# Kernel tuning notes

Hardware: AMD Instinct MI355X
Metric: run time of the kernel (lower is better)

The kernel has to match this reference:

```python
import jax, jax.numpy as jnp
import numpy as np

N = 100_000      # nodes
E = 1_600_000    # edges (avg degree 16)
IN = 512         # in_feats
HID = 4          # hidden_feats (forced equal to num_heads=4 by the mean(h,2) in forward)
H1 = 4           # heads in layer 1
OUT = 128        # out_feats
NEG_SLOPE = 0.2  # DGL GATConv leaky_relu default


def setup_inputs() -> dict:
    key = jax.random.key(0)
    ks = jax.random.split(key, 12)
    nfeats = jax.random.normal(ks[0], (N, IN), jnp.float32)
    efeats = jax.random.normal(ks[1], (E, 8), jnp.float32)  # unused by the module
    src = jax.random.randint(ks[2], (E,), 0, N, dtype=jnp.int32)
    dst = jax.random.randint(ks[3], (E,), 0, N, dtype=jnp.int32)
    # layer 1 params (in=IN, heads=H1, per-head out=HID)
    fc1_w = jax.random.normal(ks[4], (IN, H1 * HID), jnp.float32) / np.sqrt(IN)
    attn_l1 = jax.random.normal(ks[5], (H1, HID), jnp.float32) / np.sqrt(HID)
    attn_r1 = jax.random.normal(ks[6], (H1, HID), jnp.float32) / np.sqrt(HID)
    bias1 = jnp.zeros((H1 * HID,), jnp.float32)
    # layer 2 params (in=H1=4 after mean over feature dim, heads=1, out=OUT)
    fc2_w = jax.random.normal(ks[7], (HID, 1 * OUT), jnp.float32) / np.sqrt(HID)
    attn_l2 = jax.random.normal(ks[8], (1, OUT), jnp.float32) / np.sqrt(OUT)
    attn_r2 = jax.random.normal(ks[9], (1, OUT), jnp.float32) / np.sqrt(OUT)
    bias2 = jnp.zeros((OUT,), jnp.float32)
    return {"nfeats": nfeats, "efeats": efeats, "src": src, "dst": dst,
            "fc1_w": fc1_w, "attn_l1": attn_l1, "attn_r1": attn_r1, "bias1": bias1,
            "fc2_w": fc2_w, "attn_l2": attn_l2, "attn_r2": attn_r2, "bias2": bias2}


def gat_layer(x, src, dst, fc_w, attn_l, attn_r, bias, heads, d_out):
    # projection: (N, in) -> (N, H, D)
    h = (x @ fc_w).reshape(-1, heads, d_out)
    el = jnp.einsum('nhd,hd->nh', h, attn_l)   # (N, H)
    er = jnp.einsum('nhd,hd->nh', h, attn_r)
    e = jax.nn.leaky_relu(el[src] + er[dst], NEG_SLOPE)  # (E, H)
    # segment softmax over incoming edges of each dst node
    m = jax.lax.stop_gradient(jax.ops.segment_max(e, dst, num_segments=N))
    ex = jnp.exp(e - m[dst])
    denom = jax.ops.segment_sum(ex, dst, num_segments=N)
    alpha = ex / denom[dst]                    # (E, H)
    msg = alpha[:, :, None] * h[src]           # (E, H, D)
    rst = jax.ops.segment_sum(msg, dst, num_segments=N)  # (N, H, D)
    return rst + bias.reshape(1, heads, d_out)


def reference(nfeats, efeats, src, dst, fc1_w, attn_l1, attn_r1, bias1,
              fc2_w, attn_l2, attn_r2, bias2):
    h = gat_layer(nfeats, src, dst, fc1_w, attn_l1, attn_r1, bias1, H1, HID)  # (N,4,4)
    h = jnp.mean(h, axis=2)        # faithful to th.mean(h, 2): mean over per-head feat dim -> (N,4)
    h = jax.nn.relu(h)
    h = gat_layer(h, src, dst, fc2_w, attn_l2, attn_r2, bias2, 1, OUT)        # (N,1,OUT)
    return h.reshape(N, OUT)       # flatten(1)
```

## Files before the change

kernel.cpp:

```cpp
#include <hip/hip_runtime.h>
#include <math.h>

#define IN_F 512
#define OUTF 128
#define NEG_SLOPE 0.2f

typedef __attribute__((ext_vector_type(8))) short bf16x8;
typedef __attribute__((ext_vector_type(4))) float f32x4;

#define P1T 256
#define XP 136
#define NKS 16
#define BPSH 8192

#define NPB 128
#define NBMAX 784
#define EPB 4096
#define SRCMASK 0x1FFFF
#define CAP 2944

#define BP_BYTES (2 * BPSH * 2)
#define XS_BYTES (4 * 16 * XP * 2)
#define SMEM_A   (BP_BYTES + XS_BYTES)

__device__ __forceinline__ unsigned pkbf(float a, float b) {
  unsigned ua = __float_as_uint(a); ua += 0x7FFF + ((ua >> 16) & 1);
  unsigned ub = __float_as_uint(b); ub += 0x7FFF + ((ub >> 16) & 1);
  return (ua >> 16) | (ub & 0xFFFF0000u);
}

__global__ void k_prep(const float* __restrict__ fc1, const float* __restrict__ al1,
                       const float* __restrict__ ar1, const float* __restrict__ fc2,
                       const float* __restrict__ al2, const float* __restrict__ ar2,
                       unsigned short* __restrict__ BpHi, unsigned short* __restrict__ BpLo,
                       float* __restrict__ w2al, float* __restrict__ w2ar,
                       int* __restrict__ bucketCursor) {
  __shared__ float wlds[IN_F * 12];
  int t = threadIdx.x;
  if (blockIdx.x == 0) {
    int k = t;
#pragma unroll
    for (int h = 0; h < 4; ++h) {
      float wl = 0.f, wr = 0.f, wb = 0.f;
#pragma unroll
      for (int j = 0; j < 4; ++j) {
        float wv = fc1[k * 16 + h * 4 + j];
        wl = fmaf(wv, al1[h * 4 + j], wl);
        wr = fmaf(wv, ar1[h * 4 + j], wr);
        wb += wv;
      }
      wlds[k * 12 + h] = wl;
      wlds[k * 12 + 4 + h] = wr;
      wlds[k * 12 + 8 + h] = 0.25f * wb;
    }
    __syncthreads();
    for (int item = t; item < NKS * 64; item += 512) {
      int s = item >> 6, l = item & 63;
      int col = l & 15;
      int kb = s * 32 + ((l >> 4) * 8);
      unsigned hi[4], lo[4];
#pragma unroll
      for (int p = 0; p < 4; ++p) {
        float w0 = 0.f, w1 = 0.f;
        if (col < 12) {
          w0 = wlds[(kb + 2 * p) * 12 + col];
          w1 = wlds[(kb + 2 * p + 1) * 12 + col];
        }
        unsigned u0 = __float_as_uint(w0); u0 += 0x7FFF + ((u0 >> 16) & 1);
        unsigned u1 = __float_as_uint(w1); u1 += 0x7FFF + ((u1 >> 16) & 1);
        unsigned h0 = u0 >> 16, h1 = u1 >> 16;
        hi[p] = h0 | (h1 << 16);
        float r0 = w0 - __uint_as_float(h0 << 16);
        float r1 = w1 - __uint_as_float(h1 << 16);
        lo[p] = pkbf(r0, r1);
      }
      *(uint4*)&BpHi[item * 8] = make_uint4(hi[0], hi[1], hi[2], hi[3]);
      *(uint4*)&BpLo[item * 8] = make_uint4(lo[0], lo[1], lo[2], lo[3]);
    }
  } else {
    if (t < 8) {
      int h = t >> 1;
      const float* a = (t & 1) ? ar2 : al2;
      float s = 0.f;
#pragma unroll 16
      for (int c = 0; c < OUTF; ++c) s += fc2[h * OUTF + c] * a[c];
      if (t & 1) w2ar[h] = s; else w2al[h] = s;
    }
    for (int i = t; i < NBMAX; i += 512) bucketCursor[i] = 0;
  }
}

__global__ __launch_bounds__(P1T) void k_A(
    const float* __restrict__ x,
    const unsigned short* __restrict__ BpHi, const unsigned short* __restrict__ BpLo,
    float* __restrict__ pk1, float* __restrict__ er1, int n,
    const int* __restrict__ src, const int* __restrict__ dst,
    int* __restrict__ bucketCursor, unsigned* __restrict__ ep, int e,
    int projBlocks)
{
  __shared__ __align__(16) char smem[SMEM_A];
  const int t = threadIdx.x;

  if ((int)blockIdx.x < projBlocks) {
    const int lane = t & 63;
    const int wv = t >> 6;
    const bf16x8* Bfrag = (const bf16x8*)smem;
    short* xsw = (short*)(smem + BP_BYTES) + wv * (16 * XP);

    for (int i = t; i < 2 * NKS * 64; i += P1T) {
      ((uint4*)smem)[i] = (i < NKS * 64) ? ((const uint4*)BpHi)[i]
                                         : ((const uint4*)BpLo)[i - NKS * 64];
    }
    __syncthreads();

    const int totalWaves = projBlocks * 4;
    const int rtMax = (n + 15) >> 4;
    for (int rt = blockIdx.x * 4 + wv; rt < rtMax; rt += totalWaves) {
      const int wrow = rt * 16;
      const float* __restrict__ xr = x + (size_t)wrow * IN_F;
      f32x4 acc = {0.f, 0.f, 0.f, 0.f};

      float4 st[8];
#pragma unroll
      for (int i = 0; i < 8; ++i) {
        int f = lane + i * 64;
        int r = f >> 5, c4 = (f & 31) * 4;
        st[i] = (wrow + r < n) ? *(const float4*)&xr[(size_t)r * IN_F + c4]
                               : make_float4(0.f, 0.f, 0.f, 0.f);
      }

      for (int kt = 0; kt < 4; ++kt) {
#pragma unroll
        for (int i = 0; i < 8; ++i) {
          int f = lane + i * 64;
          int r = f >> 5, c4 = (f & 31) * 4;
          uint2 pv; pv.x = pkbf(st[i].x, st[i].y); pv.y = pkbf(st[i].z, st[i].w);
          *(uint2*)&xsw[r * XP + c4] = pv;
        }
        if (kt < 3) {
          int kb = (kt + 1) * 128;
#pragma unroll
          for (int i = 0; i < 8; ++i) {
            int f = lane + i * 64;
            int r = f >> 5, c4 = (f & 31) * 4;
            st[i] = (wrow + r < n) ? *(const float4*)&xr[(size_t)r * IN_F + kb + c4]
                                   : make_float4(0.f, 0.f, 0.f, 0.f);
          }
        }
        asm volatile("s_waitcnt lgkmcnt(0)" ::: "memory");
        __builtin_amdgcn_sched_barrier(0);
#pragma unroll
        for (int ks = 0; ks < 4; ++ks) {
          bf16x8 a = *(const bf16x8*)&xsw[(lane & 15) * XP + ks * 32 + ((lane >> 4) * 8)];
          int bidx = (kt * 4 + ks) * 64 + lane;
          bf16x8 bh = Bfrag[bidx];
          bf16x8 bl = Bfrag[NKS * 64 + bidx];
          acc = __builtin_amdgcn_mfma_f32_16x16x32_bf16(a, bh, acc, 0, 0, 0);
          acc = __builtin_amdgcn_mfma_f32_16x16x32_bf16(a, bl, acc, 0, 0, 0);
        }
      }

      int col = lane & 15;
      int rbase = wrow + ((lane >> 4) * 4);
#pragma unroll
      for (int i = 0; i < 4; ++i) {
        int row = rbase + i;
        if (row < n) {
          float v = acc[i];
          if (col < 4)       pk1[(size_t)row * 8 + col] = v;
          else if (col < 8)  er1[(size_t)row * 4 + (col - 4)] = v;
          else if (col < 12) pk1[(size_t)row * 8 + 4 + (col - 8)] = v;
        }
      }
    }
  } else {
    int* hist = (int*)smem;
    int* base = hist + NBMAX;
    int* lcur = base + NBMAX;
    const int bb = blockIdx.x - projBlocks;
    for (int i = t; i < NBMAX; i += P1T) hist[i] = 0;
    __syncthreads();
    int blockBase = bb * EPB;
#pragma unroll
    for (int i = 0; i < EPB / P1T; ++i) {
      int idx = blockBase + t + i * P1T;
      if (idx < e) atomicAdd(&hist[dst[idx] >> 7], 1);
    }
    __syncthreads();
    for (int i = t; i < NBMAX; i += P1T) {
      if (hist[i] > 0) base[i] = atomicAdd(&bucketCursor[i], hist[i]);
      lcur[i] = 0;
    }
    __syncthreads();
#pragma unroll
    for (int i = 0; i < EPB / P1T; ++i) {
      int idx = blockBase + t + i * P1T;
      if (idx < e) {
        int d = dst[idx];
        int b = d >> 7;
        int off = base[b] + atomicAdd(&lcur[b], 1);
        if (off < CAP)
          ep[(size_t)b * CAP + off] = (unsigned)src[idx] | ((unsigned)(d & (NPB - 1)) << 17);
      }
    }
  }
}

__global__ __launch_bounds__(256) void k_B(
    const unsigned* __restrict__ ep, const int* __restrict__ bucketCursor,
    unsigned* __restrict__ ep2, int* __restrict__ nodeBeg, int* __restrict__ nodeEnd,
    const float* __restrict__ pk1, const float* __restrict__ er1,
    const float* __restrict__ bias1,
    const float* __restrict__ w2al, const float* __restrict__ w2ar,
    float* __restrict__ pk2, float* __restrict__ er2, int n)
{
  __shared__ int cnt[NPB];
  __shared__ int scn[NPB];
  __shared__ int cur[NPB];
  __shared__ unsigned lbuf[CAP];
  int t = threadIdx.x;
  int b = blockIdx.x;
  int nodeBase = b * NPB;
  int m = bucketCursor[b];
  if (m > CAP) m = CAP;
  const unsigned* __restrict__ in = ep + (size_t)b * CAP;
  if (t < NPB) cnt[t] = 0;
  __syncthreads();
  for (int j = t; j < m; j += 256) atomicAdd(&cnt[in[j] >> 17], 1);
  __syncthreads();
  if (t < NPB) scn[t] = cnt[t];
  __syncthreads();
  for (int off = 1; off < NPB; off <<= 1) {
    int v = (t < NPB && t >= off) ? scn[t - off] : 0;
    __syncthreads();
    if (t < NPB) scn[t] += v;
    __syncthreads();
  }
  if (t < NPB) {
    int excl = scn[t] - cnt[t];
    int node = nodeBase + t;
    if (node < n) {
      nodeBeg[node] = b * CAP + excl;
      nodeEnd[node] = b * CAP + excl + cnt[t];
    }
    cur[t] = excl;
  }
  __syncthreads();
  for (int j = t; j < m; j += 256) {
    unsigned p = in[j];
    int pos = atomicAdd(&cur[p >> 17], 1);
    lbuf[pos] = p & SRCMASK;
  }
  __syncthreads();
  for (int i = t; i < m; i += 256) ep2[(size_t)b * CAP + i] = lbuf[i];

#pragma unroll
  for (int half = 0; half < 2; ++half) {
    int w = t + half * 256;
    int i = w >> 2, h = w & 3;
    int node = nodeBase + i;
    bool active = node < n;
    float v = 0.f;
    if (active) {
      int beg = scn[i] - cnt[i], end = scn[i];
      float ern = er1[(size_t)node * 4 + h];
      float den = 0.f, num = 0.f;
      for (int j = beg; j < end; ++j) {
        int s = (int)lbuf[j];
        float el = pk1[(size_t)s * 8 + h];
        float hb = pk1[(size_t)s * 8 + 4 + h];
        float eh = el + ern;
        eh = (eh > 0.f) ? eh : NEG_SLOPE * eh;
        float wg = __expf(eh);
        den += wg;
        num = fmaf(wg, hb, num);
      }
      float mb = 0.25f * (bias1[h*4] + bias1[h*4+1] + bias1[h*4+2] + bias1[h*4+3]);
      v = (end > beg) ? num / den : 0.f;
      v += mb;
      v = (v > 0.f) ? v : 0.f;
    }
    float pl = v * w2al[h];
    float pr = v * w2ar[h];
    pl += __shfl_xor(pl, 1); pl += __shfl_xor(pl, 2);
    pr += __shfl_xor(pr, 1); pr += __shfl_xor(pr, 2);
    if (active) {
      pk2[(size_t)node * 8 + h] = v;
      if (h == 0) { pk2[(size_t)node * 8 + 4] = pl; er2[node] = pr; }
    }
  }
}

__global__ __launch_bounds__(256) void k_bagg2(
    const unsigned* __restrict__ ep2, const int* __restrict__ nodeBeg,
    const int* __restrict__ nodeEnd,
    const float* __restrict__ pk2, const float* __restrict__ er2,
    const float* __restrict__ w2, const float* __restrict__ bias2,
    float* __restrict__ out, int n)
{
  __shared__ float gacc[256 * 4];
  __shared__ float w2s[4 * OUTF];
  __shared__ float b2s[OUTF];
  int t = threadIdx.x;
  int nodeBase = blockIdx.x * 256;
  int nn = nodeBase + t;
  for (int i = t; i < 4 * OUTF; i += 256) w2s[i] = w2[i];
  if (t < OUTF) b2s[t] = bias2[t];
  float g0 = 0.f, g1 = 0.f, g2 = 0.f, g3 = 0.f;
  if (nn < n) {
    int beg = nodeBeg[nn], end = nodeEnd[nn];
    float ern = er2[nn];
    float den = 0.f;
    for (int j = beg; j < end; ++j) {
      int s = (int)ep2[j];
      const float* __restrict__ ps = &pk2[(size_t)s * 8];
      float4 hv = *(const float4*)ps;
      float e = ps[4] + ern;
      e = (e > 0.f) ? e : NEG_SLOPE * e;
      float w = __expf(e);
      den += w;
      g0 = fmaf(w, hv.x, g0); g1 = fmaf(w, hv.y, g1);
      g2 = fmaf(w, hv.z, g2); g3 = fmaf(w, hv.w, g3);
    }
    float inv = (end > beg) ? 1.0f / den : 0.f;
    g0 *= inv; g1 *= inv; g2 *= inv; g3 *= inv;
  }
  gacc[t * 4 + 0] = g0; gacc[t * 4 + 1] = g1;
  gacc[t * 4 + 2] = g2; gacc[t * 4 + 3] = g3;
  __syncthreads();
  for (int idx = t; idx < 256 * (OUTF / 2); idx += 256) {
    int i = idx >> 6;
    int node = nodeBase + i;
    if (node >= n) continue;
    int c = (idx & 63) * 2;
    float gx = gacc[i*4], gy = gacc[i*4+1], gz = gacc[i*4+2], gw = gacc[i*4+3];
    float2 o;
    o.x = gx*w2s[c]   + gy*w2s[OUTF+c]   + gz*w2s[2*OUTF+c]   + gw*w2s[3*OUTF+c]   + b2s[c];
    o.y = gx*w2s[c+1] + gy*w2s[OUTF+c+1] + gz*w2s[2*OUTF+c+1] + gw*w2s[3*OUTF+c+1] + b2s[c+1];
    *(float2*)&out[(size_t)node * OUTF + c] = o;
  }
}

extern "C" void kernel_launch(void* const* d_in, const int* in_sizes, int n_in,
                              void* d_out, int out_size, void* d_ws, size_t ws_size,
                              hipStream_t stream) {
  const float* nfeats = (const float*)d_in[0];
  const int*   srcp   = (const int*)d_in[2];
  const int*   dstp   = (const int*)d_in[3];
  const float* fc1    = (const float*)d_in[4];
  const float* al1    = (const float*)d_in[5];
  const float* ar1    = (const float*)d_in[6];
  const float* bias1  = (const float*)d_in[7];
  const float* fc2    = (const float*)d_in[8];
  const float* al2    = (const float*)d_in[9];
  const float* ar2    = (const float*)d_in[10];
  const float* bias2  = (const float*)d_in[11];

  const int N = in_sizes[0] / IN_F;
  const int E = in_sizes[2];
  const int NB = (N + NPB - 1) / NPB;

  float* ws   = (float*)d_ws;
  float* pk1  = ws;
  float* er1  = pk1 + (size_t)8 * N;
  float* pk2  = er1 + (size_t)4 * N;
  float* er2  = pk2 + (size_t)8 * N;
  float* w2al = er2 + N;
  float* w2ar = w2al + 4;
  unsigned short* BpHi = (unsigned short*)(w2ar + 4);
  unsigned short* BpLo = BpHi + BPSH;
  int* bucketCursor = (int*)(BpLo + BPSH);
  int* nodeBeg      = bucketCursor + NBMAX;
  int* nodeEnd      = nodeBeg + N;
  unsigned* ep      = (unsigned*)(nodeEnd + N);
  unsigned* ep2     = ep + (size_t)NB * CAP;

  const int binBlocks = (E + EPB - 1) / EPB;
  const int projBlocks = 391;

  k_prep<<<2, 512, 0, stream>>>(fc1, al1, ar1, fc2, al2, ar2,
                                BpHi, BpLo, w2al, w2ar, bucketCursor);
  k_A<<<projBlocks + binBlocks, P1T, 0, stream>>>(nfeats, BpHi, BpLo, pk1, er1, N,
                                                  srcp, dstp, bucketCursor, ep, E,
                                                  projBlocks);
  k_B<<<NB, 256, 0, stream>>>(ep, bucketCursor, ep2, nodeBeg, nodeEnd,
                              pk1, er1, bias1, w2al, w2ar, pk2, er2, N);
  k_bagg2<<<(N + 255) / 256, 256, 0, stream>>>(ep2, nodeBeg, nodeEnd, pk2, er2,
                                               fc2, bias2, (float*)d_out, N);
}
```

Measured before the change: 135.3 us.

## Load MFMA A-fragments directly from global memory, drop LDS staging of x

The projection GEMM no longer stages converted x tiles through a per-wave LDS buffer. Each lane now loads its own 8-float slice of its row directly from global memory into registers, using a 4-deep register prefetch ring, then packs it to bf16 and feeds the MFMA. This removes the LDS writes, LDS reads and waitcnt barriers, and shrinks shared memory, which could raise occupancy. The trade-off is that global loads become less coalesced: each row is read in 32-byte pieces with a 2 KB stride between lanes instead of in contiguous rows.

New measurement: 198.1 us. +46.5%, slower.

```diff
diff --git a/kernel.cpp b/kernel.cpp
--- a/kernel.cpp
+++ b/kernel.cpp
@@ -7,10 +7,11 @@
 
 typedef __attribute__((ext_vector_type(8))) short bf16x8;
 typedef __attribute__((ext_vector_type(4))) float f32x4;
+typedef __attribute__((ext_vector_type(4))) unsigned u32x4;
 
 #define P1T 256
-#define XP 136
 #define NKS 16
+#define PFD 4
 #define BPSH 8192
 
 #define NPB 128
@@ -19,9 +20,7 @@
 #define SRCMASK 0x1FFFF
 #define CAP 2944
 
-#define BP_BYTES (2 * BPSH * 2)
-#define XS_BYTES (4 * 16 * XP * 2)
-#define SMEM_A   (BP_BYTES + XS_BYTES)
+#define SMEM_A (2 * BPSH * 2)
 
 __device__ __forceinline__ unsigned pkbf(float a, float b) {
   unsigned ua = __float_as_uint(a); ua += 0x7FFF + ((ua >> 16) & 1);
@@ -105,7 +104,6 @@
     const int lane = t & 63;
     const int wv = t >> 6;
     const bf16x8* Bfrag = (const bf16x8*)smem;
-    short* xsw = (short*)(smem + BP_BYTES) + wv * (16 * XP);
 
     for (int i = t; i < 2 * NKS * 64; i += P1T) {
       ((uint4*)smem)[i] = (i < NKS * 64) ? ((const uint4*)BpHi)[i]
@@ -113,55 +111,44 @@
     }
     __syncthreads();
 
+    const int r0 = lane & 15;
+    const int kc = (lane >> 4) * 8;
     const int totalWaves = projBlocks * 4;
     const int rtMax = (n + 15) >> 4;
+    const float4 z4 = make_float4(0.f, 0.f, 0.f, 0.f);
+
     for (int rt = blockIdx.x * 4 + wv; rt < rtMax; rt += totalWaves) {
-      const int wrow = rt * 16;
-      const float* __restrict__ xr = x + (size_t)wrow * IN_F;
+      const int myRow = rt * 16 + r0;
+      const bool ok = myRow < n;
+      const float* __restrict__ xr = x + (size_t)myRow * IN_F + kc;
       f32x4 acc = {0.f, 0.f, 0.f, 0.f};
 
-      float4 st[8];
-#pragma unroll
-      for (int i = 0; i < 8; ++i) {
-        int f = lane + i * 64;
-        int r = f >> 5, c4 = (f & 31) * 4;
-        st[i] = (wrow + r < n) ? *(const float4*)&xr[(size_t)r * IN_F + c4]
-                               : make_float4(0.f, 0.f, 0.f, 0.f);
-      }
-
-      for (int kt = 0; kt < 4; ++kt) {
-#pragma unroll
-        for (int i = 0; i < 8; ++i) {
-          int f = lane + i * 64;
-          int r = f >> 5, c4 = (f & 31) * 4;
-          uint2 pv; pv.x = pkbf(st[i].x, st[i].y); pv.y = pkbf(st[i].z, st[i].w);
-          *(uint2*)&xsw[r * XP + c4] = pv;
+      float4 q[PFD][2];
+#pragma unroll
+      for (int p = 0; p < PFD; ++p) {
+        q[p][0] = ok ? *(const float4*)&xr[p * 32] : z4;
+        q[p][1] = ok ? *(const float4*)&xr[p * 32 + 4] : z4;
+      }
+
+#pragma unroll
+      for (int ks = 0; ks < NKS; ++ks) {
+        const int slot = ks & (PFD - 1);
+        float4 a0 = q[slot][0], a1 = q[slot][1];
+        if (ks + PFD < NKS) {
+          q[slot][0] = ok ? *(const float4*)&xr[(ks + PFD) * 32] : z4;
+          q[slot][1] = ok ? *(const float4*)&xr[(ks + PFD) * 32 + 4] : z4;
         }
-        if (kt < 3) {
-          int kb = (kt + 1) * 128;
-#pragma unroll
-          for (int i = 0; i < 8; ++i) {
-            int f = lane + i * 64;
-            int r = f >> 5, c4 = (f & 31) * 4;
-            st[i] = (wrow + r < n) ? *(const float4*)&xr[(size_t)r * IN_F + kb + c4]
-                                   : make_float4(0.f, 0.f, 0.f, 0.f);
-          }
-        }
-        asm volatile("s_waitcnt lgkmcnt(0)" ::: "memory");
-        __builtin_amdgcn_sched_barrier(0);
-#pragma unroll
-        for (int ks = 0; ks < 4; ++ks) {
-          bf16x8 a = *(const bf16x8*)&xsw[(lane & 15) * XP + ks * 32 + ((lane >> 4) * 8)];
-          int bidx = (kt * 4 + ks) * 64 + lane;
-          bf16x8 bh = Bfrag[bidx];
-          bf16x8 bl = Bfrag[NKS * 64 + bidx];
-          acc = __builtin_amdgcn_mfma_f32_16x16x32_bf16(a, bh, acc, 0, 0, 0);
-          acc = __builtin_amdgcn_mfma_f32_16x16x32_bf16(a, bl, acc, 0, 0, 0);
-        }
+        u32x4 au = {pkbf(a0.x, a0.y), pkbf(a0.z, a0.w),
+                    pkbf(a1.x, a1.y), pkbf(a1.z, a1.w)};
+        union { u32x4 u; bf16x8 v; } cvt; cvt.u = au;
+        bf16x8 bh = Bfrag[ks * 64 + lane];
+        bf16x8 bl = Bfrag[NKS * 64 + ks * 64 + lane];
+        acc = __builtin_amdgcn_mfma_f32_16x16x32_bf16(cvt.v, bh, acc, 0, 0, 0);
+        acc = __builtin_amdgcn_mfma_f32_16x16x32_bf16(cvt.v, bl, acc, 0, 0, 0);
       }
 
       int col = lane & 15;
-      int rbase = wrow + ((lane >> 4) * 4);
+      int rbase = rt * 16 + ((lane >> 4) * 4);
 #pragma unroll
       for (int i = 0; i < 4; ++i) {
         int row = rbase + i;
```
